# Kernel optimization log

Hardware: AMD Instinct MI355X
Metric: run time of the kernel (lower is better)

The kernel has to match this reference:

```python
import jax, jax.numpy as jnp
import numpy as np

B, L, V, D = 4096, 128, 50257, 64
NEG_INF = -1e9
COS_EPS = 1e-8  # torch cosine_similarity default eps


def setup_inputs() -> dict:
    key = jax.random.key(0)
    k1, k2, k3, k4, k5, k6 = jax.random.split(key, 6)
    return {
        "ids_a": jax.random.randint(k1, (B, L), 0, V, dtype=jnp.int64) if jax.config.jax_enable_x64 else jax.random.randint(k1, (B, L), 0, V, dtype=jnp.int32),
        "mask_a": jax.random.randint(k2, (B, L), 0, 2, dtype=jnp.int32),
        "ids_b": jax.random.randint(k3, (B, L), 0, V, dtype=jnp.int32),
        "mask_b": jax.random.randint(k4, (B, L), 0, 2, dtype=jnp.int32),
        "mu_table": jax.random.normal(k5, (V, D), dtype=jnp.float32),
        "feat_table": jax.random.normal(k6, (V, D), dtype=jnp.float32),
    }


def _side(ids, mask, mu_table, feat_table):
    # Embedding gathers: [B, L, D]
    mu = mu_table[ids]
    feat = feat_table[ids]
    m = mask.astype(mu.dtype)  # [B, L]
    # render_mean_pool: masked mean of mu -> query [B, D]
    denom = jnp.maximum(m.sum(axis=1, keepdims=True), 1.0)
    q = jnp.einsum('bld,bl->bd', mu, m) / denom
    # render_softmax_attention: single-query masked softmax over mu keys
    scores = jnp.einsum('bld,bd->bl', mu, q)
    scores = jnp.where(mask.astype(bool), scores, NEG_INF)
    attn = jax.nn.softmax(scores, axis=-1)  # [B, L]
    return jnp.einsum('bl,bld->bd', attn, feat)  # weighted sum of feat


def reference(ids_a, mask_a, ids_b, mask_b, mu_table, feat_table):
    mean_a = _side(ids_a, mask_a, mu_table, feat_table)
    mean_b = _side(ids_b, mask_b, mu_table, feat_table)
    # torch cosine_similarity: x.y / (max(||x||, eps) * max(||y||, eps))
    na = jnp.maximum(jnp.linalg.norm(mean_a, axis=-1), COS_EPS)
    nb = jnp.maximum(jnp.linalg.norm(mean_b, axis=-1), COS_EPS)
    cos = jnp.sum(mean_a * mean_b, axis=-1) / (na * nb)
    return cos * 5.0
```

## Files before the change

### kernel.cpp

```cpp
#include <hip/hip_runtime.h>
#include <hip/hip_fp16.h>
#include <math.h>

#define BB 4096
#define LL 128
#define DD 64
#define VV 50257
#define TAB_ELEMS (VV * DD)

typedef _Float16 h2_t __attribute__((ext_vector_type(2)));

__device__ __forceinline__ float dot2acc(unsigned a, unsigned b, float c) {
#if __has_builtin(__builtin_amdgcn_fdot2)
    return __builtin_amdgcn_fdot2(__builtin_bit_cast(h2_t, a),
                                  __builtin_bit_cast(h2_t, b), c, false);
#else
    const float2 fa = __half22float2(*(const __half2*)&a);
    const float2 fb = __half22float2(*(const __half2*)&b);
    return fmaf(fa.x, fb.x, fmaf(fa.y, fb.y, c));
#endif
}

__device__ __forceinline__ float2 cvt2(unsigned raw) {
    return __half22float2(*(const __half2*)&raw);
}

__device__ __forceinline__ unsigned pack_h2(float a, float b) {
    union { __half2 h; unsigned u; } p;
    p.h = __floats2half2_rn(a, b);
    return p.u;
}

__global__ __launch_bounds__(256) void convert_tables_kernel(
    const float* __restrict__ mu, const float* __restrict__ feat,
    __half* __restrict__ out_mu, __half* __restrict__ out_feat)
{
    const int n4 = TAB_ELEMS / 4;
    for (int i = blockIdx.x * blockDim.x + threadIdx.x; i < n4;
         i += gridDim.x * blockDim.x) {
        const float4 m = ((const float4*)mu)[i];
        const float4 f = ((const float4*)feat)[i];
        uint2 pm, pf;
        pm.x = pack_h2(m.x, m.y); pm.y = pack_h2(m.z, m.w);
        pf.x = pack_h2(f.x, f.y); pf.y = pack_h2(f.z, f.w);
        ((uint2*)out_mu)[i]   = pm;
        ((uint2*)out_feat)[i] = pf;
    }
}

__global__ __launch_bounds__(256, 6) void softmax_attn_cos_kernel(
    const int* __restrict__ ids_a, const int* __restrict__ mask_a,
    const int* __restrict__ ids_b, const int* __restrict__ mask_b,
    const __half* __restrict__ mu_table, const __half* __restrict__ feat_table,
    float* __restrict__ out)
{
    __shared__ int      s_ids[2][LL];
    __shared__ float    s_msk[2][LL];
    __shared__ unsigned s_qh[2][32];
    __shared__ float4   s_qp[2][2][16];
    __shared__ float    s_sc[2][LL];
    __shared__ float4   s_op[2][2][16];
    __shared__ float    s_mean[2][DD];
    __shared__ float    s_sum[2];

    const int tid  = threadIdx.x;
    const int lane = tid & 63;
    const int wave = tid >> 6;
    const int side = wave >> 1;
    const int wsub = wave & 1;
    const int r8   = lane >> 3;
    const int c8   = lane & 7;
    const int b    = blockIdx.x;

    {
        const int si = tid >> 7;
        const int l  = tid & 127;
        const int* idp = si ? ids_b  : ids_a;
        const int* mp  = si ? mask_b : mask_a;
        s_ids[si][l] = idp[b * LL + l];
        s_msk[si][l] = (float)mp[b * LL + l];
    }
    __syncthreads();

    const unsigned long long bal =
        __ballot(s_msk[side][wsub * 64 + lane] > 0.5f);

    uint4 v[8];
    unsigned voff[8];
    unsigned kept = 0;
    {
        float4 qa = make_float4(0.f, 0.f, 0.f, 0.f);
        float4 qb = make_float4(0.f, 0.f, 0.f, 0.f);
        #pragma unroll
        for (int it = 0; it < 8; ++it) {
            const int r = wsub * 64 + it * 8 + r8;
            voff[it] = ((unsigned)s_ids[side][r] << 7) + ((unsigned)c8 << 4);
            v[it] = make_uint4(0u, 0u, 0u, 0u);
            if ((bal >> (it * 8 + r8)) & 1ull) {
                kept |= (1u << it);
                v[it] = *(const uint4*)((const char*)mu_table + voff[it]);
                const float2 f0 = cvt2(v[it].x), f1 = cvt2(v[it].y);
                const float2 f2 = cvt2(v[it].z), f3 = cvt2(v[it].w);
                qa.x += f0.x; qa.y += f0.y; qa.z += f1.x; qa.w += f1.y;
                qb.x += f2.x; qb.y += f2.y; qb.z += f3.x; qb.w += f3.y;
            }
        }
        #pragma unroll
        for (int off = 8; off <= 32; off <<= 1) {
            qa.x += __shfl_xor(qa.x, off, 64); qa.y += __shfl_xor(qa.y, off, 64);
            qa.z += __shfl_xor(qa.z, off, 64); qa.w += __shfl_xor(qa.w, off, 64);
            qb.x += __shfl_xor(qb.x, off, 64); qb.y += __shfl_xor(qb.y, off, 64);
            qb.z += __shfl_xor(qb.z, off, 64); qb.w += __shfl_xor(qb.w, off, 64);
        }
        if (lane < 8) {
            s_qp[side][wsub][2 * c8]     = qa;
            s_qp[side][wsub][2 * c8 + 1] = qb;
        }
    }
    __syncthreads();

    if (tid < 128) {
        const int si = tid >> 6;
        const int dd = tid & 63;
        float mv = s_msk[si][dd] + s_msk[si][dd + 64];
        #pragma unroll
        for (int off = 32; off; off >>= 1) mv += __shfl_xor(mv, off, 64);
        const float denom = fmaxf(mv, 1.0f);
        if (dd < 16) {
            const float4 q0 = s_qp[si][0][dd], q1 = s_qp[si][1][dd];
            const float qx = (q0.x + q1.x) / denom, qy = (q0.y + q1.y) / denom;
            const float qz = (q0.z + q1.z) / denom, qw = (q0.w + q1.w) / denom;
            s_qh[si][2 * dd]     = pack_h2(qx, qy);
            s_qh[si][2 * dd + 1] = pack_h2(qz, qw);
        }
    }
    __syncthreads();

    {
        const uint4 qq = ((const uint4*)&s_qh[side][0])[c8];
        #pragma unroll
        for (int it = 0; it < 8; ++it) {
            const int r = wsub * 64 + it * 8 + r8;
            float p = dot2acc(v[it].x, qq.x, 0.f);
            p = dot2acc(v[it].y, qq.y, p);
            p = dot2acc(v[it].z, qq.z, p);
            p = dot2acc(v[it].w, qq.w, p);
            const uint4 nf = *(const uint4*)((const char*)feat_table + voff[it]);
            #pragma unroll
            for (int off = 1; off <= 4; off <<= 1)
                p += __shfl_xor(p, off, 64);
            if (c8 == 0) s_sc[side][r] = ((kept >> it) & 1u) ? p : -1e9f;
            v[it] = nf;
        }
    }
    __syncthreads();

    if (wsub == 0) {
        const float s1 = s_sc[side][lane], s2 = s_sc[side][lane + 64];
        float mx = fmaxf(s1, s2);
        #pragma unroll
        for (int off = 32; off; off >>= 1) mx = fmaxf(mx, __shfl_xor(mx, off, 64));
        const float e1 = expf(s1 - mx), e2 = expf(s2 - mx);
        s_sc[side][lane] = e1; s_sc[side][lane + 64] = e2;
        float sm = e1 + e2;
        #pragma unroll
        for (int off = 32; off; off >>= 1) sm += __shfl_xor(sm, off, 64);
        if (lane == 0) s_sum[side] = sm;
    }
    __syncthreads();

    {
        float4 oa = make_float4(0.f, 0.f, 0.f, 0.f);
        float4 ob = make_float4(0.f, 0.f, 0.f, 0.f);
        #pragma unroll
        for (int it = 0; it < 8; ++it) {
            const int r = wsub * 64 + it * 8 + r8;
            const float w = s_sc[side][r];
            const float2 f0 = cvt2(v[it].x), f1 = cvt2(v[it].y);
            const float2 f2 = cvt2(v[it].z), f3 = cvt2(v[it].w);
            oa.x = fmaf(f0.x, w, oa.x); oa.y = fmaf(f0.y, w, oa.y);
            oa.z = fmaf(f1.x, w, oa.z); oa.w = fmaf(f1.y, w, oa.w);
            ob.x = fmaf(f2.x, w, ob.x); ob.y = fmaf(f2.y, w, ob.y);
            ob.z = fmaf(f3.x, w, ob.z); ob.w = fmaf(f3.y, w, ob.w);
        }
        #pragma unroll
        for (int off = 8; off <= 32; off <<= 1) {
            oa.x += __shfl_xor(oa.x, off, 64); oa.y += __shfl_xor(oa.y, off, 64);
            oa.z += __shfl_xor(oa.z, off, 64); oa.w += __shfl_xor(oa.w, off, 64);
            ob.x += __shfl_xor(ob.x, off, 64); ob.y += __shfl_xor(ob.y, off, 64);
            ob.z += __shfl_xor(ob.z, off, 64); ob.w += __shfl_xor(ob.w, off, 64);
        }
        if (lane < 8) {
            s_op[side][wsub][2 * c8]     = oa;
            s_op[side][wsub][2 * c8 + 1] = ob;
        }
    }
    __syncthreads();

    if (tid < 32) {
        const int si = tid >> 4, cc = tid & 15;
        const float inv = 1.0f / s_sum[si];
        const float4 o0 = s_op[si][0][cc], o1 = s_op[si][1][cc];
        float4 o;
        o.x = (o0.x + o1.x) * inv; o.y = (o0.y + o1.y) * inv;
        o.z = (o0.z + o1.z) * inv; o.w = (o0.w + o1.w) * inv;
        ((float4*)&s_mean[si][0])[cc] = o;
    }
    __syncthreads();

    if (tid < 64) {
        const float a = s_mean[0][tid], c = s_mean[1][tid];
        float dt = a * c, na = a * a, nb = c * c;
        #pragma unroll
        for (int off = 32; off; off >>= 1) {
            dt += __shfl_xor(dt, off, 64);
            na += __shfl_xor(na, off, 64);
            nb += __shfl_xor(nb, off, 64);
        }
        if (tid == 0) {
            const float denom = fmaxf(sqrtf(na), 1e-8f) * fmaxf(sqrtf(nb), 1e-8f);
            out[b] = 5.0f * dt / denom;
        }
    }
}

extern "C" void kernel_launch(void* const* d_in, const int* in_sizes, int n_in,
                              void* d_out, int out_size, void* d_ws, size_t ws_size,
                              hipStream_t stream) {
    const int*   ids_a  = (const int*)d_in[0];
    const int*   mask_a = (const int*)d_in[1];
    const int*   ids_b  = (const int*)d_in[2];
    const int*   mask_b = (const int*)d_in[3];
    const float* mu     = (const float*)d_in[4];
    const float* feat   = (const float*)d_in[5];
    float* out = (float*)d_out;

    __half* ws_mu   = (__half*)d_ws;
    __half* ws_feat = ws_mu + TAB_ELEMS;

    convert_tables_kernel<<<2048, 256, 0, stream>>>(mu, feat, ws_mu, ws_feat);
    softmax_attn_cos_kernel<<<BB, 256, 0, stream>>>(
        ids_a, mask_a, ids_b, mask_b, ws_mu, ws_feat, out);
}
```

Measured before the change: 114.0 us.

## Compact masked token ids and skip fully-masked groups of rows

Unmasked token ids are stream-compacted into shared memory with a ballot/popcount prefix, so the gather, score and weighted-sum loops cover only groups holding active tokens instead of branching per row across all 128 positions. Whole 8-row groups past the active count are skipped, which cuts divergent lanes and wasted memory instructions when about half the mask is zero. The all-masked case falls back to using every token. The cost is an extra barrier and more index bookkeeping.

```diff
diff --git a/kernel.cpp b/kernel.cpp
--- a/kernel.cpp
+++ b/kernel.cpp
@@ -54,8 +54,8 @@
     const __half* __restrict__ mu_table, const __half* __restrict__ feat_table,
     float* __restrict__ out)
 {
-    __shared__ int      s_ids[2][LL];
-    __shared__ float    s_msk[2][LL];
+    __shared__ int      s_cid[2][LL];
+    __shared__ int      s_cnt[2][2];
     __shared__ unsigned s_qh[2][32];
     __shared__ float4   s_qp[2][2][16];
     __shared__ float    s_sc[2][LL];
@@ -73,36 +73,47 @@
     const int b    = blockIdx.x;
 
     {
-        const int si = tid >> 7;
-        const int l  = tid & 127;
-        const int* idp = si ? ids_b  : ids_a;
-        const int* mp  = si ? mask_b : mask_a;
-        s_ids[si][l] = idp[b * LL + l];
-        s_msk[si][l] = (float)mp[b * LL + l];
-    }
-    __syncthreads();
-
-    const unsigned long long bal =
-        __ballot(s_msk[side][wsub * 64 + lane] > 0.5f);
+        const int l = wsub * 64 + lane;
+        const int* idp = side ? ids_b  : ids_a;
+        const int* mp  = side ? mask_b : mask_a;
+        const int id = idp[b * LL + l];
+        const int m  = mp[b * LL + l];
+        const unsigned long long bal = __ballot(m != 0);
+        if (lane == 0) s_cnt[side][wsub] = __popcll(bal);
+        const int rank = __popcll(bal & ((1ull << lane) - 1ull));
+        __syncthreads();
+        const int offset = wsub ? s_cnt[side][0] : 0;
+        if (m) s_cid[side][offset + rank] = id;
+        if (s_cnt[side][0] + s_cnt[side][1] == 0)
+            s_cid[side][l] = id;
+    }
+    __syncthreads();
+
+    const int   nm  = s_cnt[side][0] + s_cnt[side][1];
+    const int   nme = (nm == 0) ? 128 : nm;
+    const int   G   = (nme + 7) >> 3;
 
     uint4 v[8];
     unsigned voff[8];
-    unsigned kept = 0;
     {
         float4 qa = make_float4(0.f, 0.f, 0.f, 0.f);
         float4 qb = make_float4(0.f, 0.f, 0.f, 0.f);
         #pragma unroll
         for (int it = 0; it < 8; ++it) {
-            const int r = wsub * 64 + it * 8 + r8;
-            voff[it] = ((unsigned)s_ids[side][r] << 7) + ((unsigned)c8 << 4);
             v[it] = make_uint4(0u, 0u, 0u, 0u);
-            if ((bal >> (it * 8 + r8)) & 1ull) {
-                kept |= (1u << it);
+            voff[it] = 0u;
+            const int g = 2 * it + wsub;
+            if (g < G) {
+                const int p = g * 8 + r8;
+                const int id = (p < nme) ? s_cid[side][p] : 0;
+                voff[it] = ((unsigned)id << 7) + ((unsigned)c8 << 4);
                 v[it] = *(const uint4*)((const char*)mu_table + voff[it]);
-                const float2 f0 = cvt2(v[it].x), f1 = cvt2(v[it].y);
-                const float2 f2 = cvt2(v[it].z), f3 = cvt2(v[it].w);
-                qa.x += f0.x; qa.y += f0.y; qa.z += f1.x; qa.w += f1.y;
-                qb.x += f2.x; qb.y += f2.y; qb.z += f3.x; qb.w += f3.y;
+                if (p < nm) {
+                    const float2 f0 = cvt2(v[it].x), f1 = cvt2(v[it].y);
+                    const float2 f2 = cvt2(v[it].z), f3 = cvt2(v[it].w);
+                    qa.x += f0.x; qa.y += f0.y; qa.z += f1.x; qa.w += f1.y;
+                    qb.x += f2.x; qb.y += f2.y; qb.z += f3.x; qb.w += f3.y;
+                }
             }
         }
         #pragma unroll
@@ -122,16 +133,12 @@
     if (tid < 128) {
         const int si = tid >> 6;
         const int dd = tid & 63;
-        float mv = s_msk[si][dd] + s_msk[si][dd + 64];
-        #pragma unroll
-        for (int off = 32; off; off >>= 1) mv += __shfl_xor(mv, off, 64);
-        const float denom = fmaxf(mv, 1.0f);
         if (dd < 16) {
+            const float dn = fmaxf((float)(s_cnt[si][0] + s_cnt[si][1]), 1.0f);
+            const float rd = 1.0f / dn;
             const float4 q0 = s_qp[si][0][dd], q1 = s_qp[si][1][dd];
-            const float qx = (q0.x + q1.x) / denom, qy = (q0.y + q1.y) / denom;
-            const float qz = (q0.z + q1.z) / denom, qw = (q0.w + q1.w) / denom;
-            s_qh[si][2 * dd]     = pack_h2(qx, qy);
-            s_qh[si][2 * dd + 1] = pack_h2(qz, qw);
+            s_qh[si][2 * dd]     = pack_h2((q0.x + q1.x) * rd, (q0.y + q1.y) * rd);
+            s_qh[si][2 * dd + 1] = pack_h2((q0.z + q1.z) * rd, (q0.w + q1.w) * rd);
         }
     }
     __syncthreads();
@@ -140,23 +147,27 @@
         const uint4 qq = ((const uint4*)&s_qh[side][0])[c8];
         #pragma unroll
         for (int it = 0; it < 8; ++it) {
-            const int r = wsub * 64 + it * 8 + r8;
-            float p = dot2acc(v[it].x, qq.x, 0.f);
-            p = dot2acc(v[it].y, qq.y, p);
-            p = dot2acc(v[it].z, qq.z, p);
-            p = dot2acc(v[it].w, qq.w, p);
-            const uint4 nf = *(const uint4*)((const char*)feat_table + voff[it]);
-            #pragma unroll
-            for (int off = 1; off <= 4; off <<= 1)
-                p += __shfl_xor(p, off, 64);
-            if (c8 == 0) s_sc[side][r] = ((kept >> it) & 1u) ? p : -1e9f;
-            v[it] = nf;
+            const int g = 2 * it + wsub;
+            if (g < G) {
+                const int p = g * 8 + r8;
+                float sp = dot2acc(v[it].x, qq.x, 0.f);
+                sp = dot2acc(v[it].y, qq.y, sp);
+                sp = dot2acc(v[it].z, qq.z, sp);
+                sp = dot2acc(v[it].w, qq.w, sp);
+                const uint4 nf = *(const uint4*)((const char*)feat_table + voff[it]);
+                #pragma unroll
+                for (int off = 1; off <= 4; off <<= 1)
+                    sp += __shfl_xor(sp, off, 64);
+                if (c8 == 0 && p < nme) s_sc[side][p] = sp;
+                v[it] = nf;
+            }
         }
     }
     __syncthreads();
 
     if (wsub == 0) {
-        const float s1 = s_sc[side][lane], s2 = s_sc[side][lane + 64];
+        const float s1 = (lane      < nme) ? s_sc[side][lane]      : -1e9f;
+        const float s2 = (lane + 64 < nme) ? s_sc[side][lane + 64] : -1e9f;
         float mx = fmaxf(s1, s2);
         #pragma unroll
         for (int off = 32; off; off >>= 1) mx = fmaxf(mx, __shfl_xor(mx, off, 64));
@@ -174,14 +185,17 @@
         float4 ob = make_float4(0.f, 0.f, 0.f, 0.f);
         #pragma unroll
         for (int it = 0; it < 8; ++it) {
-            const int r = wsub * 64 + it * 8 + r8;
-            const float w = s_sc[side][r];
-            const float2 f0 = cvt2(v[it].x), f1 = cvt2(v[it].y);
-            const float2 f2 = cvt2(v[it].z), f3 = cvt2(v[it].w);
-            oa.x = fmaf(f0.x, w, oa.x); oa.y = fmaf(f0.y, w, oa.y);
-            oa.z = fmaf(f1.x, w, oa.z); oa.w = fmaf(f1.y, w, oa.w);
-            ob.x = fmaf(f2.x, w, ob.x); ob.y = fmaf(f2.y, w, ob.y);
-            ob.z = fmaf(f3.x, w, ob.z); ob.w = fmaf(f3.y, w, ob.w);
+            const int g = 2 * it + wsub;
+            if (g < G) {
+                const int p = g * 8 + r8;
+                const float w = (p < nme) ? s_sc[side][p] : 0.f;
+                const float2 f0 = cvt2(v[it].x), f1 = cvt2(v[it].y);
+                const float2 f2 = cvt2(v[it].z), f3 = cvt2(v[it].w);
+                oa.x = fmaf(f0.x, w, oa.x); oa.y = fmaf(f0.y, w, oa.y);
+                oa.z = fmaf(f1.x, w, oa.z); oa.w = fmaf(f1.y, w, oa.w);
+                ob.x = fmaf(f2.x, w, ob.x); ob.y = fmaf(f2.y, w, ob.y);
+                ob.z = fmaf(f3.x, w, ob.z); ob.w = fmaf(f3.y, w, ob.w);
+            }
         }
         #pragma unroll
         for (int off = 8; off <= 32; off <<= 1) {
```

After: 110.6 us (median of 2 runs). 2.9% less time.
